# Kernel optimization log

Hardware: AMD Instinct MI355X
Metric: run time of the kernel (lower is better)

The kernel has to match this reference:

```python
import jax, jax.numpy as jnp
import numpy as np

CH = 64

def _maxpool2x2(x):
    # x: [B, C, H, W] -> [B, C, H//2, W//2]
    B, C, H, W = x.shape
    return x.reshape(B, C, H // 2, 2, W // 2, 2).max(axis=(3, 5))

def _conv1x1(x, w):
    # x: [B, Cin, H, W], w: [Cout, Cin] (1x1 conv, no bias)
    return jnp.einsum('oc,bchw->bohw', w, x)

def setup_inputs() -> dict:
    key = jax.random.key(0)
    ks = jax.random.split(key, 6)
    B, H, W = 4, 128, 128
    x = jax.random.normal(ks[0], (B, CH, H, W), dtype=jnp.float32)
    # spectral-norm wrapped 1x1 conv weights; SN just rescales the weight,
    # so we materialize the (already-normalized) weight matrices directly.
    w_theta = jax.random.normal(ks[1], (CH // 8, CH), dtype=jnp.float32) * 0.05
    w_phi = jax.random.normal(ks[2], (CH // 8, CH), dtype=jnp.float32) * 0.05
    w_g = jax.random.normal(ks[3], (CH // 2, CH), dtype=jnp.float32) * 0.05
    w_o = jax.random.normal(ks[4], (CH, CH // 2), dtype=jnp.float32) * 0.05
    gamma = jnp.float32(0.5)  # nonzero so attention path contributes
    return {"x": x, "w_theta": w_theta, "w_phi": w_phi, "w_g": w_g, "w_o": w_o, "gamma": gamma}

def reference(x, w_theta, w_phi, w_g, w_o, gamma):
    B, C, H, W = x.shape
    N = H * W            # query positions
    M = (H // 2) * (W // 2)  # key/value positions after 2x2 maxpool
    theta = _conv1x1(x, w_theta).reshape(B, C // 8, N)          # [B, C/8, N]
    phi = _maxpool2x2(_conv1x1(x, w_phi)).reshape(B, C // 8, M)  # [B, C/8, M]
    g = _maxpool2x2(_conv1x1(x, w_g)).reshape(B, C // 2, M)      # [B, C/2, M]
    # beta: [B, N, M] attention over pooled key positions
    scores = jnp.einsum('bcn,bcm->bnm', theta, phi)
    beta = jax.nn.softmax(scores, axis=-1)
    # o_mid: [B, C/2, N]
    o_mid = jnp.einsum('bcm,bnm->bcn', g, beta).reshape(B, C // 2, H, W)
    o = _conv1x1(o_mid, w_o)
    return gamma * o + x
```

## Files before the change

### kernel.cpp

```cpp
#include <hip/hip_runtime.h>

typedef unsigned int uint;
typedef unsigned short ushort;
typedef __attribute__((ext_vector_type(8))) short bf16x8;
typedef __attribute__((ext_vector_type(16))) float f32x16;
typedef __attribute__((ext_vector_type(4))) uint uint4v;

constexpr int BB = 4, CHN = 64, HH = 128, WW = 128;
constexpr int NN = HH * WW;
constexpr int MM = (HH / 2) * (WW / 2);
constexpr float LOG2E = 1.44269504089f;

constexpr size_t PHI_OFF = (size_t)BB * NN * 8;
constexpr size_t GT_OFF  = PHI_OFF + (size_t)BB * MM * 8;

__device__ __forceinline__ void async16(void* lds_base, const void* gsrc) {
    __builtin_amdgcn_global_load_lds(
        (const __attribute__((address_space(1))) unsigned int*)gsrc,
        (__attribute__((address_space(3))) unsigned int*)lds_base,
        16, 0, 0);
}

__device__ __forceinline__ ushort bf16r(float f) {
    uint u = __float_as_uint(f);
    u += 0x7fff + ((u >> 16) & 1);
    return (ushort)(u >> 16);
}

__device__ __forceinline__ uint pack2(float lo, float hi) {
    return (uint)bf16r(lo) | ((uint)bf16r(hi) << 16);
}

__device__ __forceinline__ bf16x8 pack8(const float* v) {
    union { uint4v u; bf16x8 x; } cv;
    cv.u = (uint4v){pack2(v[0], v[1]), pack2(v[2], v[3]),
                    pack2(v[4], v[5]), pack2(v[6], v[7])};
    return cv.x;
}

__global__ __launch_bounds__(64)
void prep_kernel(const float* __restrict__ x,
                 const float* __restrict__ w_theta,
                 const float* __restrict__ w_phi,
                 const float* __restrict__ w_g,
                 ushort* __restrict__ theta_t,
                 ushort* __restrict__ phi_b,
                 ushort* __restrict__ gTg) {
    __shared__ float wlds[32][64];
    const int lane = threadIdx.x;
    const int part = blockIdx.y;
    float* wl = &wlds[0][0];
    if (part == 0) {
        for (int i = lane; i < 512; i += 64) wl[i] = w_theta[i] * LOG2E;
        for (int i = lane; i < 512; i += 64) wl[512 + i] = w_phi[i];
    } else {
        for (int i = lane; i < 2048; i += 64) wl[i] = w_g[i];
    }
    __syncthreads();

    const int bid = blockIdx.x;
    const int b = bid >> 8, tile = bid & 255;
    const int rp = tile >> 2, cb = tile & 3;
    const int h2 = lane >> 5, w2 = lane & 31;
    const int n = (2 * rp + h2) * WW + 32 * cb + w2;
    const float* xb = x + (size_t)b * CHN * NN + n;
    const int m = rp * 64 + 16 * cb + (w2 >> 1);

    if (part == 0) {
        float acc[16];
#pragma unroll
        for (int k = 0; k < 16; ++k) acc[k] = 0.f;
#pragma unroll 4
        for (int c = 0; c < CHN; ++c) {
            const float xv = xb[(size_t)c * NN];
#pragma unroll
            for (int k = 0; k < 16; ++k) acc[k] = fmaf(wlds[k][c], xv, acc[k]);
        }
        uint4v tv = (uint4v){pack2(acc[0], acc[1]), pack2(acc[2], acc[3]),
                             pack2(acc[4], acc[5]), pack2(acc[6], acc[7])};
        *(uint4v*)(theta_t + ((size_t)b * NN + n) * 8) = tv;
#pragma unroll
        for (int k = 8; k < 16; ++k) {
            float v = acc[k];
            v = fmaxf(v, __shfl_xor(v, 1));
            v = fmaxf(v, __shfl_xor(v, 32));
            acc[k] = v;
        }
        if (h2 == 0 && (w2 & 1) == 0) {
            uint4v pv = (uint4v){pack2(acc[8], acc[9]),   pack2(acc[10], acc[11]),
                                 pack2(acc[12], acc[13]), pack2(acc[14], acc[15])};
            *(uint4v*)(phi_b + ((size_t)b * MM + m) * 8) = pv;
        }
    } else {
        float acc[32];
#pragma unroll
        for (int k = 0; k < 32; ++k) acc[k] = 0.f;
#pragma unroll 4
        for (int c = 0; c < CHN; ++c) {
            const float xv = xb[(size_t)c * NN];
#pragma unroll
            for (int k = 0; k < 32; ++k) acc[k] = fmaf(wlds[k][c], xv, acc[k]);
        }
#pragma unroll
        for (int k = 0; k < 32; ++k) {
            float v = acc[k];
            v = fmaxf(v, __shfl_xor(v, 1));
            v = fmaxf(v, __shfl_xor(v, 32));
            acc[k] = v;
        }
        const int qidx = h2 * 2 + (w2 & 1);
        ushort* gb = gTg + (((size_t)b * (MM / 8) + (m >> 3)) * 32) * 8 + (m & 7);
#pragma unroll
        for (int j = 0; j < 8; ++j) {
            const int c = qidx * 8 + j;
            gb[(size_t)c * 8] = bf16r(acc[c]);
        }
    }
}

__global__ __launch_bounds__(256, 4)
void attn_mfma(const float* __restrict__ x,
               const ushort* __restrict__ theta_t,
               const ushort* __restrict__ phi_b,
               const ushort* __restrict__ gTg,
               const float* __restrict__ w_o,
               const float* __restrict__ gamma_p,
               float* __restrict__ out) {
    __shared__ __align__(16) ushort phiL[2][2][1024];
    __shared__ __align__(16) ushort gL[2][2][4096];

    const int tid = threadIdx.x;
    const int wv = tid >> 6, ln = tid & 63;
    const int lq = ln & 31, h = ln >> 5;
    const int ks = wv & 1, qi = wv >> 1;
    const int b = blockIdx.x >> 8;
    const int qt = blockIdx.x & 255;
    const int q0 = qt * 64 + qi * 32;

    union { uint4v u; bf16x8 v; } thc;
    thc.u = *(const uint4v*)(theta_t + ((size_t)b * NN + q0 + lq) * 8);
    const bf16x8 thB = thc.v;

    const char* phiGb = (const char*)(phi_b + (size_t)b * MM * 8);
    const char* gGb   = (const char*)(gTg + (size_t)b * MM * 32);

    f32x16 oacc, z16;
#pragma unroll
    for (int r = 0; r < 16; ++r) { oacc[r] = 0.f; z16[r] = 0.f; }
    float ssum = 0.f;

    auto stage = [&](int t, int buf) {
        for (int p = wv; p < 20; p += 4) {
            const int half = p / 10, pp = p % 10;
            if (pp < 2)
                async16(&phiL[buf][half][pp * 512],
                        phiGb + (size_t)half * 32768 + (size_t)t * 2048 + pp * 1024 + ln * 16);
            else
                async16(&gL[buf][half][(pp - 2) * 512],
                        gGb + (size_t)half * 131072 + (size_t)t * 8192 + (pp - 2) * 1024 + ln * 16);
        }
    };

    stage(0, 0);
    __syncthreads();

    for (int t = 0; t < 16; ++t) {
        const int buf = t & 1;
        if (t < 15) stage(t + 1, buf ^ 1);
        const ushort* pL = phiL[buf][ks];
        const ushort* gg = gL[buf][ks];
#pragma unroll
        for (int s = 0; s < 4; ++s) {
            bf16x8 aphi = {};
            if (h == 0) aphi = *(const bf16x8*)(pL + (s * 32 + lq) * 8);
            f32x16 S = __builtin_amdgcn_mfma_f32_32x32x16_bf16(aphi, thB, z16, 0, 0, 0);
            float e[16];
#pragma unroll
            for (int r = 0; r < 16; ++r) {
                e[r] = exp2f(fminf(S[r], 60.f));
                ssum += e[r];
            }
            uint P[8], sx[8];
#pragma unroll
            for (int i = 0; i < 8; ++i) P[i] = pack2(e[2 * i], e[2 * i + 1]);
#pragma unroll
            for (int i = 0; i < 8; ++i) sx[i] = (uint)__shfl_xor((int)P[i], 32);
            union { uint4v u; bf16x8 v; } B0c, B1c;
            B0c.u = (uint4v){h ? sx[2] : P[0], h ? sx[3] : P[1],
                             h ? P[2] : sx[0], h ? P[3] : sx[1]};
            B1c.u = (uint4v){h ? sx[6] : P[4], h ? sx[7] : P[5],
                             h ? P[6] : sx[4], h ? P[7] : sx[5]};
            const bf16x8 g0 = *(const bf16x8*)(gg + ((s * 4 + h) * 256 + lq * 8));
            const bf16x8 g1 = *(const bf16x8*)(gg + ((s * 4 + 2 + h) * 256 + lq * 8));
            oacc = __builtin_amdgcn_mfma_f32_32x32x16_bf16(g0, B0c.v, oacc, 0, 0, 0);
            oacc = __builtin_amdgcn_mfma_f32_32x32x16_bf16(g1, B1c.v, oacc, 0, 0, 0);
        }
        __syncthreads();
    }

    ssum += __shfl_xor(ssum, 32);
    float* comb = (float*)&gL[0][0][0];
    const int my = ((ks * 2 + qi) * 64 + ln) * 20;
#pragma unroll
    for (int r = 0; r < 16; ++r) comb[my + r] = oacc[r];
    comb[my + 16] = ssum;
    __syncthreads();
    const int ot = (((ks ^ 1) * 2 + qi) * 64 + ln) * 20;
#pragma unroll
    for (int r = 0; r < 16; ++r) oacc[r] += comb[ot + r];
    ssum += comb[ot + 16];

    const float sc = gamma_p[0] / fmaxf(ssum, 1e-30f);
    float o16[16];
#pragma unroll
    for (int r = 0; r < 16; ++r) o16[r] = oacc[r] * sc;
    uint OP[8], osx[8];
#pragma unroll
    for (int i = 0; i < 8; ++i) OP[i] = pack2(o16[2 * i], o16[2 * i + 1]);
#pragma unroll
    for (int i = 0; i < 8; ++i) osx[i] = (uint)__shfl_xor((int)OP[i], 32);
    union { uint4v u; bf16x8 v; } OB0c, OB1c;
    OB0c.u = (uint4v){h ? osx[2] : OP[0], h ? osx[3] : OP[1],
                      h ? OP[2] : osx[0], h ? OP[3] : osx[1]};
    OB1c.u = (uint4v){h ? osx[6] : OP[4], h ? osx[7] : OP[5],
                      h ? OP[6] : osx[4], h ? OP[7] : osx[5]};

    const float* x_b = x + (size_t)b * CHN * NN;
    float* out_b = out + (size_t)b * CHN * NN;
    const int T = ks;
    const int row = T * 32 + lq;
    const float* wr = w_o + row * 32;
    float wa[8], wb[8];
#pragma unroll
    for (int j = 0; j < 8; ++j) { wa[j] = wr[8 * h + j]; wb[j] = wr[16 + 8 * h + j]; }
    const bf16x8 A0 = pack8(wa);
    const bf16x8 A1 = pack8(wb);
    f32x16 C2 = __builtin_amdgcn_mfma_f32_32x32x16_bf16(A0, OB0c.v, z16, 0, 0, 0);
    C2 = __builtin_amdgcn_mfma_f32_32x32x16_bf16(A1, OB1c.v, C2, 0, 0, 0);
#pragma unroll
    for (int r = 0; r < 16; ++r) {
        const int oc = T * 32 + (r & 3) + 8 * (r >> 2) + 4 * h;
        const size_t idx = (size_t)oc * NN + q0 + lq;
        out_b[idx] = C2[r] + x_b[idx];
    }
}

extern "C" void kernel_launch(void* const* d_in, const int* in_sizes, int n_in,
                              void* d_out, int out_size, void* d_ws, size_t ws_size,
                              hipStream_t stream) {
    const float* x       = (const float*)d_in[0];
    const float* w_theta = (const float*)d_in[1];
    const float* w_phi   = (const float*)d_in[2];
    const float* w_g     = (const float*)d_in[3];
    const float* w_o     = (const float*)d_in[4];
    const float* gamma   = (const float*)d_in[5];
    float* out = (float*)d_out;

    ushort* theta_t = (ushort*)d_ws;
    ushort* phi_b   = theta_t + PHI_OFF;
    ushort* gTg     = theta_t + GT_OFF;

    prep_kernel<<<dim3(BB * 256, 2), dim3(64), 0, stream>>>(
        x, w_theta, w_phi, w_g, theta_t, phi_b, gTg);

    attn_mfma<<<dim3(BB * NN / 64), dim3(256), 0, stream>>>(
        x, theta_t, phi_b, gTg, w_o, gamma, out);
}
```

Before: 217.1 us.

## Permute g layout and weight order to drop cross-lane shuffles before MFMA

```diff
diff --git a/kernel.cpp b/kernel.cpp
--- a/kernel.cpp
+++ b/kernel.cpp
@@ -1,4 +1,5 @@
 #include <hip/hip_runtime.h>
+#include <hip/hip_bf16.h>
 
 typedef unsigned int uint;
 typedef unsigned short ushort;
@@ -27,14 +28,16 @@
     return (ushort)(u >> 16);
 }
 
-__device__ __forceinline__ uint pack2(float lo, float hi) {
-    return (uint)bf16r(lo) | ((uint)bf16r(hi) << 16);
-}
-
-__device__ __forceinline__ bf16x8 pack8(const float* v) {
+__device__ __forceinline__ uint pk2(float lo, float hi) {
+    union { __hip_bfloat162 h; uint u; } cv;
+    cv.h = __float22bfloat162_rn(make_float2(lo, hi));
+    return cv.u;
+}
+
+__device__ __forceinline__ bf16x8 pk8(const float* v) {
     union { uint4v u; bf16x8 x; } cv;
-    cv.u = (uint4v){pack2(v[0], v[1]), pack2(v[2], v[3]),
-                    pack2(v[4], v[5]), pack2(v[6], v[7])};
+    cv.u = (uint4v){pk2(v[0], v[1]), pk2(v[2], v[3]),
+                    pk2(v[4], v[5]), pk2(v[6], v[7])};
     return cv.x;
 }
 
@@ -47,6 +50,7 @@
                  ushort* __restrict__ phi_b,
                  ushort* __restrict__ gTg) {
     __shared__ float wlds[32][64];
+    __shared__ __align__(16) ushort stg[512];
     const int lane = threadIdx.x;
     const int part = blockIdx.y;
     float* wl = &wlds[0][0];
@@ -76,8 +80,8 @@
 #pragma unroll
             for (int k = 0; k < 16; ++k) acc[k] = fmaf(wlds[k][c], xv, acc[k]);
         }
-        uint4v tv = (uint4v){pack2(acc[0], acc[1]), pack2(acc[2], acc[3]),
-                             pack2(acc[4], acc[5]), pack2(acc[6], acc[7])};
+        uint4v tv = (uint4v){pk2(acc[0], acc[1]), pk2(acc[2], acc[3]),
+                             pk2(acc[4], acc[5]), pk2(acc[6], acc[7])};
         *(uint4v*)(theta_t + ((size_t)b * NN + n) * 8) = tv;
 #pragma unroll
         for (int k = 8; k < 16; ++k) {
@@ -87,8 +91,8 @@
             acc[k] = v;
         }
         if (h2 == 0 && (w2 & 1) == 0) {
-            uint4v pv = (uint4v){pack2(acc[8], acc[9]),   pack2(acc[10], acc[11]),
-                                 pack2(acc[12], acc[13]), pack2(acc[14], acc[15])};
+            uint4v pv = (uint4v){pk2(acc[8], acc[9]),   pk2(acc[10], acc[11]),
+                                 pk2(acc[12], acc[13]), pk2(acc[14], acc[15])};
             *(uint4v*)(phi_b + ((size_t)b * MM + m) * 8) = pv;
         }
     } else {
@@ -108,13 +112,19 @@
             v = fmaxf(v, __shfl_xor(v, 32));
             acc[k] = v;
         }
+        const int mm = w2 >> 1;
+        const int hp = (mm >> 2) & 1;
+        const int jp = (mm & 3) + 4 * ((mm >> 3) & 1);
         const int qidx = h2 * 2 + (w2 & 1);
-        ushort* gb = gTg + (((size_t)b * (MM / 8) + (m >> 3)) * 32) * 8 + (m & 7);
 #pragma unroll
         for (int j = 0; j < 8; ++j) {
             const int c = qidx * 8 + j;
-            gb[(size_t)c * 8] = bf16r(acc[c]);
-        }
+            stg[hp * 256 + c * 8 + jp] = bf16r(acc[c]);
+        }
+        const int tl = rp * 2 + (cb >> 1);
+        const int M = cb & 1;
+        uint4v val = *(uint4v*)&stg[lane * 8];
+        *(uint4v*)(gTg + ((size_t)b * (MM / 32) + tl) * 1024 + M * 512 + lane * 8) = val;
     }
 }
 
@@ -180,20 +190,12 @@
                 e[r] = exp2f(fminf(S[r], 60.f));
                 ssum += e[r];
             }
-            uint P[8], sx[8];
-#pragma unroll
-            for (int i = 0; i < 8; ++i) P[i] = pack2(e[2 * i], e[2 * i + 1]);
-#pragma unroll
-            for (int i = 0; i < 8; ++i) sx[i] = (uint)__shfl_xor((int)P[i], 32);
-            union { uint4v u; bf16x8 v; } B0c, B1c;
-            B0c.u = (uint4v){h ? sx[2] : P[0], h ? sx[3] : P[1],
-                             h ? P[2] : sx[0], h ? P[3] : sx[1]};
-            B1c.u = (uint4v){h ? sx[6] : P[4], h ? sx[7] : P[5],
-                             h ? P[6] : sx[4], h ? P[7] : sx[5]};
-            const bf16x8 g0 = *(const bf16x8*)(gg + ((s * 4 + h) * 256 + lq * 8));
-            const bf16x8 g1 = *(const bf16x8*)(gg + ((s * 4 + 2 + h) * 256 + lq * 8));
-            oacc = __builtin_amdgcn_mfma_f32_32x32x16_bf16(g0, B0c.v, oacc, 0, 0, 0);
-            oacc = __builtin_amdgcn_mfma_f32_32x32x16_bf16(g1, B1c.v, oacc, 0, 0, 0);
+            const bf16x8 B0 = pk8(e);
+            const bf16x8 B1 = pk8(e + 8);
+            const bf16x8 g0 = *(const bf16x8*)(gg + (s * 1024 + h * 256 + lq * 8));
+            const bf16x8 g1 = *(const bf16x8*)(gg + (s * 1024 + 512 + h * 256 + lq * 8));
+            oacc = __builtin_amdgcn_mfma_f32_32x32x16_bf16(g0, B0, oacc, 0, 0, 0);
+            oacc = __builtin_amdgcn_mfma_f32_32x32x16_bf16(g1, B1, oacc, 0, 0, 0);
         }
         __syncthreads();
     }
@@ -214,16 +216,8 @@
     float o16[16];
 #pragma unroll
     for (int r = 0; r < 16; ++r) o16[r] = oacc[r] * sc;
-    uint OP[8], osx[8];
-#pragma unroll
-    for (int i = 0; i < 8; ++i) OP[i] = pack2(o16[2 * i], o16[2 * i + 1]);
-#pragma unroll
-    for (int i = 0; i < 8; ++i) osx[i] = (uint)__shfl_xor((int)OP[i], 32);
-    union { uint4v u; bf16x8 v; } OB0c, OB1c;
-    OB0c.u = (uint4v){h ? osx[2] : OP[0], h ? osx[3] : OP[1],
-                      h ? OP[2] : osx[0], h ? OP[3] : osx[1]};
-    OB1c.u = (uint4v){h ? osx[6] : OP[4], h ? osx[7] : OP[5],
-                      h ? OP[6] : osx[4], h ? OP[7] : osx[5]};
+    const bf16x8 OB0 = pk8(o16);
+    const bf16x8 OB1 = pk8(o16 + 8);
 
     const float* x_b = x + (size_t)b * CHN * NN;
     float* out_b = out + (size_t)b * CHN * NN;
@@ -232,11 +226,15 @@
     const float* wr = w_o + row * 32;
     float wa[8], wb[8];
 #pragma unroll
-    for (int j = 0; j < 8; ++j) { wa[j] = wr[8 * h + j]; wb[j] = wr[16 + 8 * h + j]; }
-    const bf16x8 A0 = pack8(wa);
-    const bf16x8 A1 = pack8(wb);
-    f32x16 C2 = __builtin_amdgcn_mfma_f32_32x32x16_bf16(A0, OB0c.v, z16, 0, 0, 0);
-    C2 = __builtin_amdgcn_mfma_f32_32x32x16_bf16(A1, OB1c.v, C2, 0, 0, 0);
+    for (int j = 0; j < 8; ++j) {
+        const int ch = 8 * (j >> 2) + 4 * h + (j & 3);
+        wa[j] = wr[ch];
+        wb[j] = wr[16 + ch];
+    }
+    const bf16x8 A0 = pk8(wa);
+    const bf16x8 A1 = pk8(wb);
+    f32x16 C2 = __builtin_amdgcn_mfma_f32_32x32x16_bf16(A0, OB0, z16, 0, 0, 0);
+    C2 = __builtin_amdgcn_mfma_f32_32x32x16_bf16(A1, OB1, C2, 0, 0, 0);
 #pragma unroll
     for (int r = 0; r < 16; ++r) {
         const int oc = T * 32 + (r & 3) + 8 * (r >> 2) + 4 * h;
```

Result: faster. 206.0 us (-5.1%).
